# Optimization experiments

Hardware: AMD Instinct MI355X
Metric: run time of the kernel (lower is better)

Reference implementation:

```python
import jax, jax.numpy as jnp
import numpy as np

B, D_IN, U, M = 8192, 512, 256, 50  # batch, input_size, num_units(=v_size), max_n_msgs


def _w(key, shape, scale=0.02):
    return (jax.random.normal(key, shape, dtype=jnp.float32) * scale)


def setup_inputs() -> dict:
    key = jax.random.key(0)
    ks = jax.random.split(key, 32)
    inp = {
        "X": jax.random.normal(ks[0], (B, D_IN), dtype=jnp.float32),
        "S": jax.random.normal(ks[1], (B, M, U), dtype=jnp.float32),
        "h": jax.random.normal(ks[2], (B, U), dtype=jnp.float32),
        "v": jax.random.normal(ks[3], (B, U), dtype=jnp.float32),
        # attention params
        "W_sa": _w(ks[4], (U, U)), "W_ha": _w(ks[5], (U, U)),
        "b_a": jnp.zeros((U,), jnp.float32), "v_a": _w(ks[6], (U,)),
        # gates
        "W_f": _w(ks[7], (U, U)), "W_hf": _w(ks[8], (U, U)), "b_f": jnp.zeros((U,), jnp.float32),
        "W_o": _w(ks[9], (U, U)), "W_ho": _w(ks[10], (U, U)), "b_o": jnp.zeros((U,), jnp.float32),
        "W_t": _w(ks[11], (U, U)), "W_ht": _w(ks[12], (U, U)), "b_t": jnp.zeros((U,), jnp.float32),
        "W_k": _w(ks[13], (D_IN, U)), "W_hk": _w(ks[14], (U, U)), "W_vk": _w(ks[15], (U, U)), "b_k": jnp.zeros((U,), jnp.float32),
        "W_s": _w(ks[16], (D_IN, U)), "W_hs": _w(ks[17], (U, U)), "b_s": jnp.zeros((U,), jnp.float32),
        "W_v": _w(ks[18], (U, U)), "W_hv": _w(ks[19], (U, U)), "b_v": jnp.zeros((U,), jnp.float32),
    }
    return inp


def reference(X, S, h, v,
              W_sa, W_ha, b_a, v_a,
              W_f, W_hf, b_f,
              W_o, W_ho, b_o,
              W_t, W_ht, b_t,
              W_k, W_hk, W_vk, b_k,
              W_s, W_hs, b_s,
              W_v, W_hv, b_v):
    # additive attention over messages: a [B, M, U]
    a = jnp.tanh(jnp.einsum('bmv,vu->bmu', S, W_sa) + (h @ W_ha + b_a)[:, None, :])
    scores = jnp.einsum('bmu,u->bm', a, v_a)            # [B, M]
    P = jax.nn.softmax(scores, axis=1)                  # [B, M]
    text = jnp.einsum('bm,bmv->bv', P, S)               # [B, U]
    # LSTM-like gates
    F = jax.nn.sigmoid(text @ W_f + h @ W_hf + b_f)
    O = jax.nn.sigmoid(text @ W_o + h @ W_ho + b_o)
    text_new = jnp.tanh(text @ W_t + h @ W_ht + b_t)
    V = F * v + O * text_new                            # [B, U]
    k = jax.nn.sigmoid(X @ W_k + h @ W_hk + V @ W_vk + b_k)
    hx = jnp.tanh(X @ W_s + h @ W_hs + b_s)
    hv = jnp.tanh(V @ W_v + h @ W_hv + b_v)
    H = (1.0 - k) * hv + k * hx                         # [B, U]
    # original returns (H, P, MSINStateTuple(H, V)); new_state.h == H
    return (H, P, V)
```

## Files before the change

### kernel.cpp

```cpp
#include <hip/hip_runtime.h>
#include <cstddef>

typedef __bf16 bf16x8 __attribute__((ext_vector_type(8)));
typedef unsigned short u16x8 __attribute__((ext_vector_type(8)));
typedef float f32x4 __attribute__((ext_vector_type(4)));

#define B_N 8192
#define M_N 50
#define R_N (B_N * M_N)
#define P_OFF ((size_t)B_N * 256)
#define V_OFF ((size_t)B_N * 256 + (size_t)B_N * 50)

__device__ __forceinline__ float bf2f(unsigned short u) {
  return __uint_as_float(((unsigned int)u) << 16);
}
__device__ __forceinline__ unsigned short f2bf(float f) {
  unsigned int u = __float_as_uint(f);
  u += 0x7fffu + ((u >> 16) & 1u);
  return (unsigned short)(u >> 16);
}
__device__ __forceinline__ float fsig(float x) { return 1.f / (1.f + __expf(-x)); }
__device__ __forceinline__ float ftanh(float x) {
  float e = __expf(2.f * x);
  return 1.f - 2.f / (e + 1.f);
}

__device__ __forceinline__ float ld_ext(const void* p, size_t i, bool f32) {
  return f32 ? ((const float*)p)[i] : bf2f(((const unsigned short*)p)[i]);
}

__device__ __forceinline__ void gload_lds16(const void* g, void* l) {
  __builtin_amdgcn_global_load_lds(
      (const __attribute__((address_space(1))) unsigned int*)g,
      (__attribute__((address_space(3))) unsigned int*)l, 16, 0, 0);
}

__device__ __forceinline__ unsigned swz(unsigned a) {
  return a ^ (((a >> 7) & 7u) << 4);
}

__global__ void probe_dtype(const void* __restrict__ X, int* __restrict__ flag) {
  const int lane = threadIdx.x;
  const unsigned short u = ((const unsigned short*)X)[lane * 2];
  const int e = (u >> 7) & 0xff;
  const bool plausible = (e >= 110 && e <= 144) || (u == 0);
  const unsigned long long m = __ballot(plausible);
  if (lane == 0) *flag = (__popcll(m) < 32) ? 1 : 0;
}

struct TJobs {
  const void* src[15];
  unsigned short* dst[15];
  int K[15];
};

__global__ __launch_bounds__(256) void transpose_weights(TJobs jobs, const int* __restrict__ flagp) {
  const bool f32 = *flagp != 0;
  const int z = blockIdx.z;
  const void* __restrict__ src = jobs.src[z];
  unsigned short* __restrict__ dst = jobs.dst[z];
  const int K = jobs.K[z];
  const int k0 = blockIdx.y * 16;
  if (k0 >= K) return;
  const int n0 = blockIdx.x * 16;
  __shared__ __align__(16) unsigned short tile[16][17];
  const int tx = threadIdx.x & 15, ty = threadIdx.x >> 4;
  const size_t sidx = (size_t)(k0 + ty) * 256 + n0 + tx;
  tile[ty][tx] = f32 ? f2bf(((const float*)src)[sidx]) : ((const unsigned short*)src)[sidx];
  __syncthreads();
  dst[(size_t)(n0 + ty) * K + k0 + tx] = tile[tx][ty];
}

struct GJob {
  const void* A[3];
  const unsigned short* Wt[3];
  int K[3];
  int atag[3];
  const void* bias;
  const unsigned short* add;
  unsigned short* out;
  int act;
};
struct GJobs { GJob j[4]; };

__global__ __launch_bounds__(256) void gemm_small(GJobs jobs, const int* __restrict__ flagp) {
  const bool flag32 = *flagp != 0;
  const GJob job = jobs.j[blockIdx.z];
  const int tid = threadIdx.x;
  const int row0 = blockIdx.x * 64;
  const int col0 = blockIdx.y * 128;
  __shared__ __align__(16) unsigned short As[2][64][40];
  __shared__ __align__(16) unsigned short Ws[2][128][40];

  f32x4 acc[2][4];
#pragma unroll
  for (int i = 0; i < 2; ++i)
#pragma unroll
    for (int j = 0; j < 4; ++j) acc[i][j] = (f32x4){0.f, 0.f, 0.f, 0.f};

  const int wave = tid >> 6, lane = tid & 63;
  const int wr = wave >> 1, wc = wave & 1;
  const int quad = lane >> 4, l16 = lane & 15;

  const void* Aseg[3]; const unsigned short* Wseg[3]; int Kseg[3]; bool Fseg[3];
  int nseg = 0, nt = 0, sbeg[4];
  sbeg[0] = 0;
  for (int p = 0; p < 3; ++p) {
    if (job.K[p] == 0) break;
    Aseg[nseg] = job.A[p]; Wseg[nseg] = job.Wt[p]; Kseg[nseg] = job.K[p];
    Fseg[nseg] = (job.atag[p] == 1) || (job.atag[p] == 2 && flag32);
    nt += job.K[p] / 32;
    ++nseg; sbeg[nseg] = nt;
  }

  const int rA = tid >> 2, cA = (tid & 3) * 8;
  const int rW = tid >> 2, cW = (tid & 3) * 8;

  uint4 pa, pw0, pw1;
  float4 fa, fb;
  bool pf32 = false;

  auto issue = [&](int t) {
    int s = 0;
    while (t >= sbeg[s + 1]) ++s;
    const int k0 = (t - sbeg[s]) * 32;
    const int Kp = Kseg[s];
    pf32 = Fseg[s];
    if (pf32) {
      const float* fp = (const float*)Aseg[s] + (size_t)(row0 + rA) * Kp + k0 + cA;
      fa = *(const float4*)fp;
      fb = *(const float4*)(fp + 4);
    } else {
      pa = *(const uint4*)((const unsigned short*)Aseg[s] + (size_t)(row0 + rA) * Kp + k0 + cA);
    }
    pw0 = *(const uint4*)&Wseg[s][(size_t)(col0 + rW) * Kp + k0 + cW];
    pw1 = *(const uint4*)&Wseg[s][(size_t)(col0 + rW + 64) * Kp + k0 + cW];
  };
  auto commit = [&](int buf) {
    if (pf32) {
      u16x8 v;
      v[0] = f2bf(fa.x); v[1] = f2bf(fa.y); v[2] = f2bf(fa.z); v[3] = f2bf(fa.w);
      v[4] = f2bf(fb.x); v[5] = f2bf(fb.y); v[6] = f2bf(fb.z); v[7] = f2bf(fb.w);
      *(u16x8*)&As[buf][rA][cA] = v;
    } else {
      *(uint4*)&As[buf][rA][cA] = pa;
    }
    *(uint4*)&Ws[buf][rW][cW] = pw0;
    *(uint4*)&Ws[buf][rW + 64][cW] = pw1;
  };

  issue(0);
  commit(0);
  __syncthreads();

  int buf = 0;
  for (int t = 0; t < nt; ++t) {
    if (t + 1 < nt) issue(t + 1);
    bf16x8 af[2], bfr[4];
#pragma unroll
    for (int mi = 0; mi < 2; ++mi)
      af[mi] = *(const bf16x8*)&As[buf][wr * 32 + mi * 16 + l16][quad * 8];
#pragma unroll
    for (int ni = 0; ni < 4; ++ni)
      bfr[ni] = *(const bf16x8*)&Ws[buf][wc * 64 + ni * 16 + l16][quad * 8];
#pragma unroll
    for (int mi = 0; mi < 2; ++mi)
#pragma unroll
      for (int ni = 0; ni < 4; ++ni)
        acc[mi][ni] = __builtin_amdgcn_mfma_f32_16x16x32_bf16(af[mi], bfr[ni], acc[mi][ni], 0, 0, 0);
    if (t + 1 < nt) commit(buf ^ 1);
    __syncthreads();
    buf ^= 1;
  }

#pragma unroll
  for (int mi = 0; mi < 2; ++mi) {
#pragma unroll
    for (int ni = 0; ni < 4; ++ni) {
      const int col = col0 + wc * 64 + ni * 16 + l16;
      const float bias = job.bias ? ld_ext(job.bias, col, flag32) : 0.f;
      const int rowb = row0 + wr * 32 + mi * 16 + quad * 4;
#pragma unroll
      for (int r = 0; r < 4; ++r) {
        float v = acc[mi][ni][r] + bias;
        const size_t idx = (size_t)(rowb + r) * 256 + col;
        if (job.add) v += bf2f(job.add[idx]);
        if (job.act == 1) v = fsig(v);
        else if (job.act == 2) v = ftanh(v);
        job.out[idx] = f2bf(v);
      }
    }
  }
}

__global__ __launch_bounds__(512, 4) void attn_fused(
    const void* __restrict__ S,
    const unsigned short* __restrict__ WsaT,
    const unsigned short* __restrict__ hWa,
    const void* __restrict__ v_a,
    float* __restrict__ out,
    unsigned short* __restrict__ text,
    const int* __restrict__ flagp) {
  const bool f32 = *flagp != 0;
  const int tid = threadIdx.x;
  const int b0 = blockIdx.x;
  const size_t srow0 = (size_t)b0 * 50;

  __shared__ __align__(128) unsigned short Sl[8 * 64 * 32];
  __shared__ __align__(128) unsigned short Wl[2 * 256 * 32];
  __shared__ float hWs[256];
  __shared__ float vas[256];
  __shared__ __align__(16) float red[64][4];
  __shared__ float Pl[64];

  const int wave = tid >> 6, lane = tid & 63;
  const int wr = wave >> 2, wc = wave & 3;
  const int quad = lane >> 4, l16 = lane & 15;

  const unsigned cS = (unsigned)tid * 16;
  const unsigned lS = swz(cS);
  const unsigned rowS = lS >> 6;
  const unsigned eS = (lS & 63) >> 1;
  const size_t gS = (srow0 + (rowS < 50 ? rowS : 49)) * 256 + eS;

  const unsigned c0 = (unsigned)tid * 16, c1 = c0 + 8192;
  const unsigned l0 = swz(c0), l1 = swz(c1);
  const size_t gW0 = (size_t)(l0 >> 6) * 256 + ((l0 & 63) >> 1);
  const size_t gW1 = (size_t)(l1 >> 6) * 256 + ((l1 & 63) >> 1);

  auto stageS = [&](int t) {
    if (wave < 4) {
      if (f32) {
        const float* fp = (const float*)S + gS + t * 32;
        const float4 a = *(const float4*)fp;
        const float4 b = *(const float4*)(fp + 4);
        u16x8 v;
        v[0] = f2bf(a.x); v[1] = f2bf(a.y); v[2] = f2bf(a.z); v[3] = f2bf(a.w);
        v[4] = f2bf(b.x); v[5] = f2bf(b.y); v[6] = f2bf(b.z); v[7] = f2bf(b.w);
        *(u16x8*)((char*)Sl + t * 4096 + cS) = v;
      } else {
        gload_lds16((const unsigned short*)S + gS + t * 32,
                    (char*)Sl + t * 4096 + (wave << 10));
      }
    }
  };
  auto stageW = [&](int t, int buf) {
    char* base = (char*)Wl + buf * 16384;
    gload_lds16(WsaT + gW0 + t * 32, base + (wave << 10));
    gload_lds16(WsaT + gW1 + t * 32, base + 8192 + (wave << 10));
  };

  f32x4 acc[2][4];
#pragma unroll
  for (int i = 0; i < 2; ++i)
#pragma unroll
    for (int j = 0; j < 4; ++j) acc[i][j] = (f32x4){0.f, 0.f, 0.f, 0.f};

  stageS(0);
  stageW(0, 0);
  if (tid < 256) {
    hWs[tid] = bf2f(hWa[(size_t)b0 * 256 + tid]);
    vas[tid] = ld_ext(v_a, tid, f32);
  }
  __syncthreads();

  for (int t = 0; t < 8; ++t) {
    if (t < 7) { stageS(t + 1); stageW(t + 1, (t + 1) & 1); }
    const char* sl = (const char*)Sl + t * 4096;
    const char* wl = (const char*)Wl + (t & 1) * 16384;
    bf16x8 af[2], bfr[4];
#pragma unroll
    for (int mi = 0; mi < 2; ++mi)
      af[mi] = *(const bf16x8*)(sl + swz((unsigned)(wr * 32 + mi * 16 + l16) * 64 + quad * 16));
#pragma unroll
    for (int ni = 0; ni < 4; ++ni)
      bfr[ni] = *(const bf16x8*)(wl + swz((unsigned)(wc * 64 + ni * 16 + l16) * 64 + quad * 16));
#pragma unroll
    for (int mi = 0; mi < 2; ++mi)
#pragma unroll
      for (int ni = 0; ni < 4; ++ni)
        acc[mi][ni] = __builtin_amdgcn_mfma_f32_16x16x32_bf16(af[mi], bfr[ni], acc[mi][ni], 0, 0, 0);
    __syncthreads();
  }

#pragma unroll
  for (int mi = 0; mi < 2; ++mi) {
#pragma unroll
    for (int r = 0; r < 4; ++r) {
      const int rl = wr * 32 + mi * 16 + quad * 4 + r;
      float s = 0.f;
#pragma unroll
      for (int ni = 0; ni < 4; ++ni) {
        const int col = wc * 64 + ni * 16 + l16;
        s += ftanh(acc[mi][ni][r] + hWs[col]) * vas[col];
      }
      s += __shfl_xor(s, 1);
      s += __shfl_xor(s, 2);
      s += __shfl_xor(s, 4);
      s += __shfl_xor(s, 8);
      if (l16 == 0) red[rl][wc] = s;
    }
  }
  __syncthreads();

  if (tid < 64) {
    const float4 rr = *(const float4*)&red[tid][0];
    const float sc = rr.x + rr.y + rr.z + rr.w;
    float sv = (tid < 50) ? sc : -1e30f;
    float mx = sv;
#pragma unroll
    for (int off = 32; off > 0; off >>= 1) mx = fmaxf(mx, __shfl_xor(mx, off));
    float e = (tid < 50) ? __expf(sv - mx) : 0.f;
    float sum = e;
#pragma unroll
    for (int off = 32; off > 0; off >>= 1) sum += __shfl_xor(sum, off);
    const float p = e / sum;
    Pl[tid] = p;
    if (tid < 50) out[P_OFF + (size_t)b0 * 50 + tid] = p;
  }
  __syncthreads();

  if (tid < 256) {
    const int t = tid >> 5;
    const unsigned bc = (unsigned)(tid & 31) * 2;
    float a = 0.f;
#pragma unroll 10
    for (int m = 0; m < 50; ++m) {
      const unsigned off = (unsigned)t * 4096 + swz((unsigned)m * 64 + bc);
      a += Pl[m] * bf2f(*(const unsigned short*)((const char*)Sl + off));
    }
    text[(size_t)b0 * 256 + tid] = f2bf(a);
  }
}

__global__ __launch_bounds__(256) void v_combine(
    const unsigned short* __restrict__ F, const unsigned short* __restrict__ O,
    const unsigned short* __restrict__ T,
    const void* __restrict__ v, float* __restrict__ out,
    const int* __restrict__ flagp) {
  const bool f32 = *flagp != 0;
  const int i = (blockIdx.x * 256 + threadIdx.x) * 4;
  float v0, v1, v2, v3;
  if (f32) {
    const float4 vv = *(const float4*)((const float*)v + i);
    v0 = vv.x; v1 = vv.y; v2 = vv.z; v3 = vv.w;
  } else {
    const uint2 vr = *(const uint2*)((const unsigned short*)v + i);
    v0 = bf2f((unsigned short)(vr.x & 0xffffu));
    v1 = bf2f((unsigned short)(vr.x >> 16));
    v2 = bf2f((unsigned short)(vr.y & 0xffffu));
    v3 = bf2f((unsigned short)(vr.y >> 16));
  }
  const uint2 Fr = *(const uint2*)&F[i];
  const uint2 Or = *(const uint2*)&O[i];
  const uint2 Tr = *(const uint2*)&T[i];
  float4 o;
  o.x = bf2f((unsigned short)(Fr.x & 0xffffu)) * v0 + bf2f((unsigned short)(Or.x & 0xffffu)) * bf2f((unsigned short)(Tr.x & 0xffffu));
  o.y = bf2f((unsigned short)(Fr.x >> 16))     * v1 + bf2f((unsigned short)(Or.x >> 16))     * bf2f((unsigned short)(Tr.x >> 16));
  o.z = bf2f((unsigned short)(Fr.y & 0xffffu)) * v2 + bf2f((unsigned short)(Or.y & 0xffffu)) * bf2f((unsigned short)(Tr.y & 0xffffu));
  o.w = bf2f((unsigned short)(Fr.y >> 16))     * v3 + bf2f((unsigned short)(Or.y >> 16))     * bf2f((unsigned short)(Tr.y >> 16));
  *(float4*)&out[V_OFF + i] = o;
}

__global__ __launch_bounds__(256) void h_combine(
    const unsigned short* __restrict__ kk, const unsigned short* __restrict__ hv,
    const unsigned short* __restrict__ hx, float* __restrict__ Hout) {
  const int i = (blockIdx.x * 256 + threadIdx.x) * 4;
  const uint2 kr = *(const uint2*)&kk[i];
  const uint2 vr = *(const uint2*)&hv[i];
  const uint2 xr = *(const uint2*)&hx[i];
  const float k0 = bf2f((unsigned short)(kr.x & 0xffffu)), k1 = bf2f((unsigned short)(kr.x >> 16));
  const float k2 = bf2f((unsigned short)(kr.y & 0xffffu)), k3 = bf2f((unsigned short)(kr.y >> 16));
  const float hv0 = bf2f((unsigned short)(vr.x & 0xffffu)), hv1 = bf2f((unsigned short)(vr.x >> 16));
  const float hv2 = bf2f((unsigned short)(vr.y & 0xffffu)), hv3 = bf2f((unsigned short)(vr.y >> 16));
  const float hx0 = bf2f((unsigned short)(xr.x & 0xffffu)), hx1 = bf2f((unsigned short)(xr.x >> 16));
  const float hx2 = bf2f((unsigned short)(xr.y & 0xffffu)), hx3 = bf2f((unsigned short)(xr.y >> 16));
  float4 o;
  o.x = (1.f - k0) * hv0 + k0 * hx0;
  o.y = (1.f - k1) * hv1 + k1 * hx1;
  o.z = (1.f - k2) * hv2 + k2 * hx2;
  o.w = (1.f - k3) * hv3 + k3 * hx3;
  *(float4*)&Hout[i] = o;
}

extern "C" void kernel_launch(void* const* d_in, const int* in_sizes, int n_in,
                              void* d_out, int out_size, void* d_ws, size_t ws_size,
                              hipStream_t stream) {
  const void* X   = d_in[0];
  const void* S   = d_in[1];
  const void* h   = d_in[2];
  const void* v   = d_in[3];
  const void* b_a = d_in[6];
  const void* v_a = d_in[7];
  const void* b_f = d_in[10];
  const void* b_o = d_in[13];
  const void* b_t = d_in[16];
  const void* b_k = d_in[20];
  const void* b_s = d_in[23];
  const void* b_v = d_in[26];

  float* out = (float*)d_out;
  float* out_V = out + V_OFF;

  char* ws = (char*)d_ws;
  int* flag = (int*)ws;
  size_t off = 256;

  const int widx[15] = {4, 5, 8, 9, 11, 12, 14, 15, 17, 18, 19, 21, 22, 24, 25};
  const int wK[15]   = {256, 256, 256, 256, 256, 256, 256, 256, 512, 256, 256, 512, 256, 256, 256};
  TJobs tj;
  unsigned short* wt[15];
  for (int i = 0; i < 15; ++i) {
    wt[i] = (unsigned short*)(ws + off);
    off += (size_t)wK[i] * 256 * 2;
    tj.src[i] = d_in[widx[i]];
    tj.dst[i] = wt[i];
    tj.K[i] = wK[i];
  }
  const unsigned short *WsaT = wt[0], *WhaT = wt[1], *WfT = wt[2], *WhfT = wt[3],
                       *WoT = wt[4], *WhoT = wt[5], *WtT = wt[6], *WhtT = wt[7],
                       *WkT = wt[8], *WhkT = wt[9], *WvkT = wt[10], *WsT = wt[11],
                       *WhsT = wt[12], *WvT = wt[13], *WhvT = wt[14];
  off = (off + 255) & ~(size_t)255;
  const size_t BS = (size_t)B_N * 256 * 2;
  unsigned short* hWa   = (unsigned short*)(ws + off); off += BS;
  unsigned short* text  = (unsigned short*)(ws + off); off += BS;
  unsigned short* Fb    = (unsigned short*)(ws + off); off += BS;
  unsigned short* Ob    = (unsigned short*)(ws + off); off += BS;
  unsigned short* Tb    = (unsigned short*)(ws + off); off += BS;
  unsigned short* kpre  = (unsigned short*)(ws + off); off += BS;
  unsigned short* hx    = (unsigned short*)(ws + off); off += BS;
  unsigned short* hvpre = (unsigned short*)(ws + off); off += BS;

  probe_dtype<<<1, 64, 0, stream>>>(X, flag);
  transpose_weights<<<dim3(16, 32, 15), 256, 0, stream>>>(tj, flag);

  GJobs jA;
  for (int i = 0; i < 4; ++i) jA.j[i] = GJob{};
  jA.j[0].A[0] = h;  jA.j[0].atag[0] = 2; jA.j[0].Wt[0] = WhaT; jA.j[0].K[0] = 256;
  jA.j[0].bias = b_a; jA.j[0].out = hWa; jA.j[0].act = 0;
  jA.j[1].A[0] = X;  jA.j[1].atag[0] = 2; jA.j[1].Wt[0] = WkT;  jA.j[1].K[0] = 512;
  jA.j[1].A[1] = h;  jA.j[1].atag[1] = 2; jA.j[1].Wt[1] = WhkT; jA.j[1].K[1] = 256;
  jA.j[1].bias = b_k; jA.j[1].out = kpre; jA.j[1].act = 0;
  jA.j[2].A[0] = X;  jA.j[2].atag[0] = 2; jA.j[2].Wt[0] = WsT;  jA.j[2].K[0] = 512;
  jA.j[2].A[1] = h;  jA.j[2].atag[1] = 2; jA.j[2].Wt[1] = WhsT; jA.j[2].K[1] = 256;
  jA.j[2].bias = b_s; jA.j[2].out = hx; jA.j[2].act = 2;
  jA.j[3].A[0] = h;  jA.j[3].atag[0] = 2; jA.j[3].Wt[0] = WhvT; jA.j[3].K[0] = 256;
  jA.j[3].bias = b_v; jA.j[3].out = hvpre; jA.j[3].act = 0;
  gemm_small<<<dim3(128, 2, 4), 256, 0, stream>>>(jA, flag);

  attn_fused<<<dim3(B_N), 512, 0, stream>>>(S, WsaT, hWa, v_a, out, text, flag);

  GJobs jB;
  for (int i = 0; i < 4; ++i) jB.j[i] = GJob{};
  jB.j[0].A[0] = text; jB.j[0].atag[0] = 0; jB.j[0].Wt[0] = WfT;  jB.j[0].K[0] = 256;
  jB.j[0].A[1] = h;    jB.j[0].atag[1] = 2; jB.j[0].Wt[1] = WhfT; jB.j[0].K[1] = 256;
  jB.j[0].bias = b_f; jB.j[0].out = Fb; jB.j[0].act = 1;
  jB.j[1].A[0] = text; jB.j[1].atag[0] = 0; jB.j[1].Wt[0] = WoT;  jB.j[1].K[0] = 256;
  jB.j[1].A[1] = h;    jB.j[1].atag[1] = 2; jB.j[1].Wt[1] = WhoT; jB.j[1].K[1] = 256;
  jB.j[1].bias = b_o; jB.j[1].out = Ob; jB.j[1].act = 1;
  jB.j[2].A[0] = text; jB.j[2].atag[0] = 0; jB.j[2].Wt[0] = WtT;  jB.j[2].K[0] = 256;
  jB.j[2].A[1] = h;    jB.j[2].atag[1] = 2; jB.j[2].Wt[1] = WhtT; jB.j[2].K[1] = 256;
  jB.j[2].bias = b_t; jB.j[2].out = Tb; jB.j[2].act = 2;
  gemm_small<<<dim3(128, 2, 3), 256, 0, stream>>>(jB, flag);

  v_combine<<<dim3(B_N * 256 / 1024), 256, 0, stream>>>(Fb, Ob, Tb, v, out, flag);

  GJobs jC;
  for (int i = 0; i < 4; ++i) jC.j[i] = GJob{};
  jC.j[0].A[0] = out_V; jC.j[0].atag[0] = 1; jC.j[0].Wt[0] = WvkT; jC.j[0].K[0] = 256;
  jC.j[0].add = kpre; jC.j[0].out = kpre; jC.j[0].act = 1;
  jC.j[1].A[0] = out_V; jC.j[1].atag[0] = 1; jC.j[1].Wt[0] = WvT;  jC.j[1].K[0] = 256;
  jC.j[1].add = hvpre; jC.j[1].out = hvpre; jC.j[1].act = 2;
  gemm_small<<<dim3(128, 2, 2), 256, 0, stream>>>(jC, flag);

  h_combine<<<dim3(B_N * 256 / 1024), 256, 0, stream>>>(kpre, hvpre, hx, out);
}
```

Measured before the change: 858.2 us.

## Make attention kernel persistent over 16 batches with register-resident W_sa

The attention kernel now processes 16 batch rows per block instead of one. Each wave keeps its 32-column slice of W_sa in registers for the whole block rather than restaging W through LDS every k-step. The next batch's S tile is double-buffered into LDS while the current one is computed. The text weighted-sum is split across all 512 threads in two halves. This cuts repeated weight loads and per-block launch overhead, at the cost of higher register pressure, a grid of only 512 blocks, and more barriers per batch.

Result: no change. 870.3 us (+1.4%).

```diff
diff --git a/kernel.cpp b/kernel.cpp
--- a/kernel.cpp
+++ b/kernel.cpp
@@ -10,6 +10,8 @@
 #define R_N (B_N * M_N)
 #define P_OFF ((size_t)B_N * 256)
 #define V_OFF ((size_t)B_N * 256 + (size_t)B_N * 50)
+#define NBAT 16
+#define NBLK (B_N / NBAT)
 
 __device__ __forceinline__ float bf2f(unsigned short u) {
   return __uint_as_float(((unsigned int)u) << 16);
@@ -203,133 +205,126 @@
     const int* __restrict__ flagp) {
   const bool f32 = *flagp != 0;
   const int tid = threadIdx.x;
-  const int b0 = blockIdx.x;
-  const size_t srow0 = (size_t)b0 * 50;
-
-  __shared__ __align__(128) unsigned short Sl[8 * 64 * 32];
-  __shared__ __align__(128) unsigned short Wl[2 * 256 * 32];
-  __shared__ float hWs[256];
-  __shared__ float vas[256];
-  __shared__ __align__(16) float red[64][4];
+  const int wave = tid >> 6, lane = tid & 63;
+  const int quad = lane >> 4, l16 = lane & 15;
+  const int col0 = wave * 32;
+
+  __shared__ __align__(128) unsigned short Sl[2][8 * 64 * 32];
+  __shared__ __align__(16) float red[64][8];
   __shared__ float Pl[64];
-
-  const int wave = tid >> 6, lane = tid & 63;
-  const int wr = wave >> 2, wc = wave & 3;
-  const int quad = lane >> 4, l16 = lane & 15;
-
-  const unsigned cS = (unsigned)tid * 16;
-  const unsigned lS = swz(cS);
-  const unsigned rowS = lS >> 6;
-  const unsigned eS = (lS & 63) >> 1;
-  const size_t gS = (srow0 + (rowS < 50 ? rowS : 49)) * 256 + eS;
-
-  const unsigned c0 = (unsigned)tid * 16, c1 = c0 + 8192;
-  const unsigned l0 = swz(c0), l1 = swz(c1);
-  const size_t gW0 = (size_t)(l0 >> 6) * 256 + ((l0 & 63) >> 1);
-  const size_t gW1 = (size_t)(l1 >> 6) * 256 + ((l1 & 63) >> 1);
-
-  auto stageS = [&](int t) {
-    if (wave < 4) {
+  __shared__ __align__(16) float tpart[2][256];
+
+  bf16x8 wf[8][2];
+#pragma unroll
+  for (int kk = 0; kk < 8; ++kk)
+#pragma unroll
+    for (int ni = 0; ni < 2; ++ni)
+      wf[kk][ni] = *(const bf16x8*)&WsaT[(size_t)(col0 + ni * 16 + l16) * 256 + kk * 32 + quad * 8];
+
+  const float va0 = ld_ext(v_a, col0 + l16, f32);
+  const float va1 = ld_ext(v_a, col0 + 16 + l16, f32);
+
+  const int b0 = blockIdx.x * NBAT;
+
+  auto stage = [&](int b, int buf) {
+#pragma unroll
+    for (int i = 0; i < 4; ++i) {
+      const unsigned c = (unsigned)tid * 16 + i * 8192;
+      const unsigned sl = c >> 12;
+      const unsigned l = swz(c & 4095);
+      const unsigned row = l >> 6;
+      const unsigned ke = sl * 32 + ((l & 63) >> 1);
+      const size_t g = ((size_t)b * 50 + (row < 50 ? row : 49)) * 256 + ke;
       if (f32) {
-        const float* fp = (const float*)S + gS + t * 32;
+        const float* fp = (const float*)S + g;
         const float4 a = *(const float4*)fp;
-        const float4 b = *(const float4*)(fp + 4);
+        const float4 bb = *(const float4*)(fp + 4);
         u16x8 v;
         v[0] = f2bf(a.x); v[1] = f2bf(a.y); v[2] = f2bf(a.z); v[3] = f2bf(a.w);
-        v[4] = f2bf(b.x); v[5] = f2bf(b.y); v[6] = f2bf(b.z); v[7] = f2bf(b.w);
-        *(u16x8*)((char*)Sl + t * 4096 + cS) = v;
+        v[4] = f2bf(bb.x); v[5] = f2bf(bb.y); v[6] = f2bf(bb.z); v[7] = f2bf(bb.w);
+        *(u16x8*)((char*)Sl[buf] + c) = v;
       } else {
-        gload_lds16((const unsigned short*)S + gS + t * 32,
-                    (char*)Sl + t * 4096 + (wave << 10));
+        gload_lds16((const unsigned short*)S + g,
+                    (char*)Sl[buf] + (wave << 10) + i * 8192);
       }
     }
   };
-  auto stageW = [&](int t, int buf) {
-    char* base = (char*)Wl + buf * 16384;
-    gload_lds16(WsaT + gW0 + t * 32, base + (wave << 10));
-    gload_lds16(WsaT + gW1 + t * 32, base + 8192 + (wave << 10));
-  };
-
-  f32x4 acc[2][4];
-#pragma unroll
-  for (int i = 0; i < 2; ++i)
-#pragma unroll
-    for (int j = 0; j < 4; ++j) acc[i][j] = (f32x4){0.f, 0.f, 0.f, 0.f};
-
-  stageS(0);
-  stageW(0, 0);
-  if (tid < 256) {
-    hWs[tid] = bf2f(hWa[(size_t)b0 * 256 + tid]);
-    vas[tid] = ld_ext(v_a, tid, f32);
-  }
+
+  stage(b0, 0);
   __syncthreads();
 
-  for (int t = 0; t < 8; ++t) {
-    if (t < 7) { stageS(t + 1); stageW(t + 1, (t + 1) & 1); }
-    const char* sl = (const char*)Sl + t * 4096;
-    const char* wl = (const char*)Wl + (t & 1) * 16384;
-    bf16x8 af[2], bfr[4];
-#pragma unroll
-    for (int mi = 0; mi < 2; ++mi)
-      af[mi] = *(const bf16x8*)(sl + swz((unsigned)(wr * 32 + mi * 16 + l16) * 64 + quad * 16));
-#pragma unroll
-    for (int ni = 0; ni < 4; ++ni)
-      bfr[ni] = *(const bf16x8*)(wl + swz((unsigned)(wc * 64 + ni * 16 + l16) * 64 + quad * 16));
-#pragma unroll
-    for (int mi = 0; mi < 2; ++mi)
-#pragma unroll
-      for (int ni = 0; ni < 4; ++ni)
-        acc[mi][ni] = __builtin_amdgcn_mfma_f32_16x16x32_bf16(af[mi], bfr[ni], acc[mi][ni], 0, 0, 0);
+  for (int bi = 0; bi < NBAT; ++bi) {
+    const int b = b0 + bi;
+    const int buf = bi & 1;
+    if (bi + 1 < NBAT) stage(b + 1, buf ^ 1);
+
+    const float hw0 = bf2f(hWa[(size_t)b * 256 + col0 + l16]);
+    const float hw1 = bf2f(hWa[(size_t)b * 256 + col0 + 16 + l16]);
+
+    const char* sl = (const char*)Sl[buf];
+    f32x4 acc[4][2];
+#pragma unroll
+    for (int mi = 0; mi < 4; ++mi) {
+      acc[mi][0] = (f32x4){0.f, 0.f, 0.f, 0.f};
+      acc[mi][1] = (f32x4){0.f, 0.f, 0.f, 0.f};
+    }
+#pragma unroll
+    for (int kk = 0; kk < 8; ++kk) {
+#pragma unroll
+      for (int mi = 0; mi < 4; ++mi) {
+        const bf16x8 af = *(const bf16x8*)(sl + kk * 4096 +
+                              swz((unsigned)(mi * 16 + l16) * 64 + quad * 16));
+        acc[mi][0] = __builtin_amdgcn_mfma_f32_16x16x32_bf16(af, wf[kk][0], acc[mi][0], 0, 0, 0);
+        acc[mi][1] = __builtin_amdgcn_mfma_f32_16x16x32_bf16(af, wf[kk][1], acc[mi][1], 0, 0, 0);
+      }
+    }
+
+#pragma unroll
+    for (int mi = 0; mi < 4; ++mi) {
+#pragma unroll
+      for (int r = 0; r < 4; ++r) {
+        float s = ftanh(acc[mi][0][r] + hw0) * va0 + ftanh(acc[mi][1][r] + hw1) * va1;
+        s += __shfl_xor(s, 1);
+        s += __shfl_xor(s, 2);
+        s += __shfl_xor(s, 4);
+        s += __shfl_xor(s, 8);
+        if (l16 == 0) red[mi * 16 + quad * 4 + r][wave] = s;
+      }
+    }
     __syncthreads();
-  }
-
-#pragma unroll
-  for (int mi = 0; mi < 2; ++mi) {
-#pragma unroll
-    for (int r = 0; r < 4; ++r) {
-      const int rl = wr * 32 + mi * 16 + quad * 4 + r;
-      float s = 0.f;
-#pragma unroll
-      for (int ni = 0; ni < 4; ++ni) {
-        const int col = wc * 64 + ni * 16 + l16;
-        s += ftanh(acc[mi][ni][r] + hWs[col]) * vas[col];
-      }
-      s += __shfl_xor(s, 1);
-      s += __shfl_xor(s, 2);
-      s += __shfl_xor(s, 4);
-      s += __shfl_xor(s, 8);
-      if (l16 == 0) red[rl][wc] = s;
-    }
-  }
-  __syncthreads();
-
-  if (tid < 64) {
-    const float4 rr = *(const float4*)&red[tid][0];
-    const float sc = rr.x + rr.y + rr.z + rr.w;
-    float sv = (tid < 50) ? sc : -1e30f;
-    float mx = sv;
-#pragma unroll
-    for (int off = 32; off > 0; off >>= 1) mx = fmaxf(mx, __shfl_xor(mx, off));
-    float e = (tid < 50) ? __expf(sv - mx) : 0.f;
-    float sum = e;
-#pragma unroll
-    for (int off = 32; off > 0; off >>= 1) sum += __shfl_xor(sum, off);
-    const float p = e / sum;
-    Pl[tid] = p;
-    if (tid < 50) out[P_OFF + (size_t)b0 * 50 + tid] = p;
-  }
-  __syncthreads();
-
-  if (tid < 256) {
-    const int t = tid >> 5;
-    const unsigned bc = (unsigned)(tid & 31) * 2;
-    float a = 0.f;
-#pragma unroll 10
-    for (int m = 0; m < 50; ++m) {
-      const unsigned off = (unsigned)t * 4096 + swz((unsigned)m * 64 + bc);
-      a += Pl[m] * bf2f(*(const unsigned short*)((const char*)Sl + off));
-    }
-    text[(size_t)b0 * 256 + tid] = f2bf(a);
+
+    if (tid < 64) {
+      const float4* rp = (const float4*)red[tid];
+      const float4 x = rp[0], y = rp[1];
+      const float sc = x.x + x.y + x.z + x.w + y.x + y.y + y.z + y.w;
+      float sv = (tid < 50) ? sc : -1e30f;
+      float mx = sv;
+#pragma unroll
+      for (int off = 32; off > 0; off >>= 1) mx = fmaxf(mx, __shfl_xor(mx, off));
+      float e = (tid < 50) ? __expf(sv - mx) : 0.f;
+      float sum = e;
+#pragma unroll
+      for (int off = 32; off > 0; off >>= 1) sum += __shfl_xor(sum, off);
+      const float p = e / sum;
+      Pl[tid] = p;
+      if (tid < 50) out[P_OFF + (size_t)b * 50 + tid] = p;
+    }
+    __syncthreads();
+
+    {
+      const int col = tid & 255, hh = tid >> 8;
+      const unsigned slice = (unsigned)(col >> 5) * 4096;
+      const unsigned bc = (unsigned)(col & 31) * 2;
+      float a = 0.f;
+      const int m0 = hh * 25;
+#pragma unroll 5
+      for (int m = m0; m < m0 + 25; ++m)
+        a += Pl[m] * bf2f(*(const unsigned short*)(sl + slice + swz((unsigned)m * 64 + bc)));
+      tpart[hh][col] = a;
+    }
+    __syncthreads();
+    if (tid < 256)
+      text[(size_t)b * 256 + tid] = f2bf(tpart[0][tid] + tpart[1][tid]);
   }
 }
 
@@ -449,7 +444,7 @@
   jA.j[3].bias = b_v; jA.j[3].out = hvpre; jA.j[3].act = 0;
   gemm_small<<<dim3(128, 2, 4), 256, 0, stream>>>(jA, flag);
 
-  attn_fused<<<dim3(B_N), 512, 0, stream>>>(S, WsaT, hWa, v_a, out, text, flag);
+  attn_fused<<<dim3(NBLK), 512, 0, stream>>>(S, WsaT, hWa, v_a, out, text, flag);
 
   GJobs jB;
   for (int i = 0; i < 4; ++i) jB.j[i] = GJob{};
```
